# Optimization experiments

Measured on AMD Instinct MI355X. Metric: run time of the kernel, lower is better.

The kernel has to match this reference:

```python
import jax, jax.numpy as jnp
import numpy as np


def setup_inputs() -> dict:
    key = jax.random.key(0)
    k1, k2, k3, k4 = jax.random.split(key, 4)
    B, H, S, E, L = 2, 12, 256, 64, 25
    return {
        "attention_probs": jax.random.uniform(k1, (B, H, S, S), dtype=jnp.float32),
        "value_attentions": jax.random.normal(k2, (B, H, S, E), dtype=jnp.float32),
        "relative_positions": jax.random.normal(k3, (B, S, S, H * E), dtype=jnp.float32),
        "W": jax.random.normal(k4, (L, H * E), dtype=jnp.float32) * 0.02,
        "b": jnp.zeros((L,), dtype=jnp.float32),
    }


def reference(attention_probs, value_attentions, relative_positions, W, b):
    # Faithful translation of TransformerMHSLayer.forward:
    #   out[b,h,i,j,e] = p[b,h,i,j] * (v[b,h,j,e] + rel[b,i,j,h,e])
    #   pre[b,j,i,l]   = sum_{h,e} out[b,h,i,j,e] * W[l, h*E+e] + bias[l]
    #   logits[b,j,l,i] = pre[b,j,i,l]
    B, H, S, E = value_attentions.shape
    L = W.shape[0]
    Wr = W.reshape(L, H, E)                       # [L,H,E], matches h*E+e flattening
    rel = relative_positions.reshape(B, S, S, H, E)  # view(B,S,S,H,E)
    # value term: contract v with W per head, then weight by attention probs
    pre = jnp.einsum('bhij,bhje,lhe->bjil', attention_probs, value_attentions, Wr)
    # relative-position term (same attention weighting)
    pre = pre + jnp.einsum('bhij,bijhe,lhe->bjil', attention_probs, rel, Wr)
    pre = pre + b                                  # bias over label dim
    return pre.transpose(0, 1, 3, 2)               # [B, S(j), L, S(i)]
```

## Files before the change

### kernel.cpp

```cpp
#include <hip/hip_runtime.h>
#include <stdint.h>


#define Bb 2
#define Hh 12
#define Ss 256
#define Ee 64
#define Ll 25
#define Kk 768

#define JT 4
#define NR 16
#define CHF 256
#define RSTR 268
#define BUFF (NR * RSTR)
#define REDF 2048
#define NUNIT (JT * 3)

typedef __attribute__((ext_vector_type(8))) short bf16x8;
typedef __attribute__((ext_vector_type(4))) float f32x4;

#define NFRAG (Hh * 4)
#define AB_BYTES ((size_t)NFRAG * 64 * 8 * 2)
#define PT_BYTES ((size_t)Bb * Ss * Hh * Ss * 4)
#define WV_BYTES ((size_t)Bb * Ss * Hh * 32 * 4)

typedef const void __attribute__((address_space(1)))* gas_ptr;
typedef void __attribute__((address_space(3)))* las_ptr;

__device__ __forceinline__ void async_copy16(void* lds_dst, const void* g_src) {
    __builtin_amdgcn_global_load_lds((gas_ptr)g_src, (las_ptr)lds_dst, 16, 0, 0);
}

__device__ __forceinline__ ushort f2bf(float x) {
    union { float f; uint32_t u; } u; u.f = x;
    uint32_t r = u.u + 0x7fff + ((u.u >> 16) & 1);
    return (ushort)(r >> 16);
}

__global__ void a_pack_kernel(const float* __restrict__ W, ushort* __restrict__ ab) {
    int idx = blockIdx.x * 256 + threadIdx.x;
    if (idx >= NFRAG * 64) return;
    int lane = idx & 63, fi = idx >> 6;
    int Lt = fi & 1, ks = (fi >> 1) & 1, h = fi >> 2;
    int l = Lt * 16 + (lane & 15);
    int k0 = h * Ee + ks * 32 + (lane >> 4) * 8;
    ushort* dst = ab + (size_t)idx * 8;
#pragma unroll
    for (int t = 0; t < 8; ++t)
        dst[t] = (l < Ll) ? f2bf(W[l * Kk + k0 + t]) : (ushort)0;
}

__global__ void p_transpose_kernel(const float* __restrict__ p,
                                   float* __restrict__ pt) {
    __shared__ float tile[32][33];
    const int bh = blockIdx.y;
    const int b = bh / Hh, h = bh % Hh;
    const int ti = blockIdx.x >> 3, tj = blockIdx.x & 7;
    const int tx = threadIdx.x & 31, ty = threadIdx.x >> 5;
#pragma unroll
    for (int s = 0; s < 4; ++s) {
        const int il = ty + 8 * s;
        tile[il][tx] = p[((size_t)(b * Hh + h) * Ss + ti * 32 + il) * Ss + tj * 32 + tx];
    }
    __syncthreads();
#pragma unroll
    for (int s = 0; s < 4; ++s) {
        const int jl = ty + 8 * s;
        pt[((size_t)(b * Ss + tj * 32 + jl) * Hh + h) * Ss + ti * 32 + tx] = tile[tx][jl];
    }
}

__global__ void wv_kernel(const float* __restrict__ W, const float* __restrict__ v,
                          float* __restrict__ wv) {
    const int bj = blockIdx.x;
    const int b = bj >> 8, j = bj & (Ss - 1);
    const int t = threadIdx.x;
    const int h = t >> 5, l = t & 31;
    float acc = 0.f;
    if (l < Ll) {
        const float* wrow = W + l * Kk + h * Ee;
        const float* vrow = v + ((size_t)(b * Hh + h) * Ss + j) * Ee;
#pragma unroll
        for (int e = 0; e < Ee; ++e) acc = __builtin_fmaf(wrow[e], vrow[e], acc);
    }
    wv[((size_t)bj * Hh + h) * 32 + l] = acc;
}

__global__ __launch_bounds__(256, 3) void mhs_lds(
    const float* __restrict__ pt,
    const float* __restrict__ rel,
    const ushort* __restrict__ ab,
    const float* __restrict__ wv,
    const float* __restrict__ bias,
    float* __restrict__ out)
{
    __shared__ __align__(16) float lds[2 * BUFF + REDF];

    const int n = blockIdx.x;
    const int jt = n & 63, it = (n >> 6) & 15, b = n >> 10;
    const int j0 = jt * JT, i0 = it * NR;
    const int tid = threadIdx.x;
    const int w = tid >> 6, lane = tid & 63;
    const int col = lane & 15, grp = lane >> 4;

    auto stage = [&](int u, int d) {
        const int jj = u / 3, c = u - jj * 3;
#pragma unroll
        for (int q = 0; q < 4; ++q) {
            const int row = w * 4 + q;
            const float* src = rel
                + ((size_t)(b * Ss + i0 + row) * Ss + (j0 + jj)) * Kk
                + c * CHF + lane * 4;
            async_copy16(&lds[d * BUFF + row * RSTR], src);
        }
    };

    f32x4 acc0 = {0.f, 0.f, 0.f, 0.f};
    f32x4 acc1 = {0.f, 0.f, 0.f, 0.f};

    stage(0, 0);
    int buf = 0;
#pragma unroll 1
    for (int u = 0; u < NUNIT; ++u) {
        __syncthreads();
        if (u + 1 < NUNIT) stage(u + 1, buf ^ 1);

        const int jj = u / 3, c = u - jj * 3;
        const int j = j0 + jj;
        const int h = c * 4 + w;

        const ushort* ap = ab + (size_t)h * 2048 + lane * 8;
        const bf16x8 A00 = *(const bf16x8*)(ap);
        const bf16x8 A01 = *(const bf16x8*)(ap + 512);
        const bf16x8 A10 = *(const bf16x8*)(ap + 1024);
        const bf16x8 A11 = *(const bf16x8*)(ap + 1536);

        const float pv = pt[((size_t)(b * Ss + j) * Hh + h) * Ss + i0 + col];

        const float* rb = &lds[buf * BUFF + col * RSTR + w * 64 + grp * 8];
        const float4 x0 = *(const float4*)(rb);
        const float4 x1 = *(const float4*)(rb + 4);
        const float4 y0 = *(const float4*)(rb + 32);
        const float4 y1 = *(const float4*)(rb + 36);

        bf16x8 B0, B1;
#pragma unroll
        for (int t = 0; t < 4; ++t) {
            B0[t]     = (short)f2bf(pv * ((const float*)&x0)[t]);
            B0[t + 4] = (short)f2bf(pv * ((const float*)&x1)[t]);
            B1[t]     = (short)f2bf(pv * ((const float*)&y0)[t]);
            B1[t + 4] = (short)f2bf(pv * ((const float*)&y1)[t]);
        }
        acc0 = __builtin_amdgcn_mfma_f32_16x16x32_bf16(A00, B0, acc0, 0, 0, 0);
        acc0 = __builtin_amdgcn_mfma_f32_16x16x32_bf16(A10, B1, acc0, 0, 0, 0);
        acc1 = __builtin_amdgcn_mfma_f32_16x16x32_bf16(A01, B0, acc1, 0, 0, 0);
        acc1 = __builtin_amdgcn_mfma_f32_16x16x32_bf16(A11, B1, acc1, 0, 0, 0);

        if (c == 2) {
#pragma unroll
            for (int hh = 0; hh < 3; ++hh) {
                const int h2 = hh * 4 + w;
                const float pvh = pt[((size_t)(b * Ss + j) * Hh + h2) * Ss + i0 + col];
                const float* wp = wv + ((size_t)(b * Ss + j) * Hh + h2) * 32 + grp * 4;
                const f32x4 w0 = *(const f32x4*)(wp);
                const f32x4 w1 = *(const f32x4*)(wp + 16);
                acc0 += pvh * w0;
                acc1 += pvh * w1;
            }
            float* red = &lds[2 * BUFF];
#pragma unroll
            for (int r = 0; r < 4; ++r) {
                red[w * 512 + (grp * 4 + r) * 16 + col]        = acc0[r];
                red[w * 512 + (16 + grp * 4 + r) * 16 + col]   = acc1[r];
            }
            __syncthreads();
#pragma unroll
            for (int ss = 0; ss < 2; ++ss) {
                const int s = tid + ss * 256;
                const int lp = s >> 4, cc = s & 15;
                if (lp < Ll) {
                    const float val = red[s] + red[512 + s] + red[1024 + s]
                                    + red[1536 + s] + bias[lp];
                    out[((size_t)(b * Ss + j) * Ll + lp) * Ss + i0 + cc] = val;
                }
            }
            acc0 = (f32x4){0.f, 0.f, 0.f, 0.f};
            acc1 = (f32x4){0.f, 0.f, 0.f, 0.f};
        }
        buf ^= 1;
    }
}

__global__ __launch_bounds__(256, 4) void mhs_basic(
    const float* __restrict__ p, const float* __restrict__ v,
    const float* __restrict__ rel, const float* __restrict__ W,
    const float* __restrict__ bias, float* __restrict__ out)
{
    const int g = blockIdx.x;
    const int ig = g & 3, j = (g >> 2) & (Ss - 1), b = g >> 10;
    const int tid = threadIdx.x;
    const int w = tid >> 6, lane = tid & 63;
    const int col = lane & 15, grp = lane >> 4;
    const int iw = ig * 64 + w * 16 + col;
    const float* relp = rel + ((size_t)(b * Ss + iw) * Ss + j) * Kk + grp * 8;

    f32x4 acc0 = {0.f, 0.f, 0.f, 0.f}, acc1 = {0.f, 0.f, 0.f, 0.f};
#pragma unroll 1
    for (int h = 0; h < Hh; ++h) {
        bf16x8 A00, A01, A10, A11;
#pragma unroll
        for (int t = 0; t < 8; ++t) {
            const int kb = h * Ee + grp * 8 + t;
            const int la = col, lb = 16 + col;
            A00[t] = (short)f2bf(W[la * Kk + kb]);
            A01[t] = (lb < Ll) ? (short)f2bf(W[lb * Kk + kb]) : (short)0;
            A10[t] = (short)f2bf(W[la * Kk + kb + 32]);
            A11[t] = (lb < Ll) ? (short)f2bf(W[lb * Kk + kb + 32]) : (short)0;
        }
        const float* vbp = v + ((size_t)(b * Hh + h) * Ss + j) * Ee + grp * 8;
        const float4 va0 = *(const float4*)(vbp);
        const float4 va1 = *(const float4*)(vbp + 4);
        const float4 vc0 = *(const float4*)(vbp + 32);
        const float4 vc1 = *(const float4*)(vbp + 36);
        const float* rb = relp + h * Ee;
        const float4 c0 = *(const float4*)(rb);
        const float4 c1 = *(const float4*)(rb + 4);
        const float4 c2 = *(const float4*)(rb + 32);
        const float4 c3 = *(const float4*)(rb + 36);
        const float pv = p[((size_t)(b * Hh + h) * Ss + iw) * Ss + j];
        bf16x8 B0, B1;
#pragma unroll
        for (int t = 0; t < 4; ++t) {
            B0[t]     = (short)f2bf(pv * (((const float*)&c0)[t] + ((const float*)&va0)[t]));
            B0[t + 4] = (short)f2bf(pv * (((const float*)&c1)[t] + ((const float*)&va1)[t]));
            B1[t]     = (short)f2bf(pv * (((const float*)&c2)[t] + ((const float*)&vc0)[t]));
            B1[t + 4] = (short)f2bf(pv * (((const float*)&c3)[t] + ((const float*)&vc1)[t]));
        }
        acc0 = __builtin_amdgcn_mfma_f32_16x16x32_bf16(A00, B0, acc0, 0, 0, 0);
        acc0 = __builtin_amdgcn_mfma_f32_16x16x32_bf16(A10, B1, acc0, 0, 0, 0);
        acc1 = __builtin_amdgcn_mfma_f32_16x16x32_bf16(A01, B0, acc1, 0, 0, 0);
        acc1 = __builtin_amdgcn_mfma_f32_16x16x32_bf16(A11, B1, acc1, 0, 0, 0);
    }
#pragma unroll
    for (int r = 0; r < 4; ++r) {
        const int l0 = grp * 4 + r;
        out[((size_t)(b * Ss + j) * Ll + l0) * Ss + iw] = acc0[r] + bias[l0];
        const int l1 = 16 + grp * 4 + r;
        if (l1 < Ll)
            out[((size_t)(b * Ss + j) * Ll + l1) * Ss + iw] = acc1[r] + bias[l1];
    }
}

extern "C" void kernel_launch(void* const* d_in, const int* in_sizes, int n_in,
                              void* d_out, int out_size, void* d_ws, size_t ws_size,
                              hipStream_t stream) {
    const float* p    = (const float*)d_in[0];
    const float* v    = (const float*)d_in[1];
    const float* rel  = (const float*)d_in[2];
    const float* W    = (const float*)d_in[3];
    const float* bias = (const float*)d_in[4];
    float* out = (float*)d_out;

    const bool full = ws_size >= AB_BYTES + PT_BYTES + WV_BYTES;

    if (full) {
        ushort* ab = (ushort*)d_ws;
        float* pt  = (float*)((char*)d_ws + AB_BYTES);
        float* wvp = (float*)((char*)d_ws + AB_BYTES + PT_BYTES);
        hipLaunchKernelGGL(a_pack_kernel, dim3((NFRAG * 64 + 255) / 256), dim3(256),
                           0, stream, W, ab);
        hipLaunchKernelGGL(p_transpose_kernel, dim3(64, Bb * Hh), dim3(256),
                           0, stream, p, pt);
        hipLaunchKernelGGL(wv_kernel, dim3(Bb * Ss), dim3(Hh * 32),
                           0, stream, W, v, wvp);
        hipLaunchKernelGGL(mhs_lds, dim3(Bb * 16 * 64), dim3(256), 0, stream,
                           pt, rel, ab, wvp, bias, out);
    } else {
        hipLaunchKernelGGL(mhs_basic, dim3(Bb * Ss * 4), dim3(256), 0, stream,
                           p, v, rel, W, bias, out);
    }
}
```

Before: 125.1 us.

## Deepen rel prefetch pipeline with register-prefetched operands and explicit waitcnt barriers

Restructures the main loop so the rel tile is staged two units ahead, and the A fragments, p value and wv vectors for the next unit are loaded into registers during the current one. Block syncs become raw s_barrier calls with manual vmcnt/lgkmcnt waits. The value-term fold is spread across each head's unit instead of being done in a burst at the reduction, and the bias loads are hoisted out of the loop. The LDS row stride shrinks from 268 to 260, which may change bank conflicts. The reduction code contains dead leftover expressions, and the hand-written waitcnt counts tie correctness to the exact number of outstanding loads.

```diff
diff --git a/kernel.cpp b/kernel.cpp
--- a/kernel.cpp
+++ b/kernel.cpp
@@ -12,7 +12,7 @@
 #define JT 4
 #define NR 16
 #define CHF 256
-#define RSTR 268
+#define RSTR 260
 #define BUFF (NR * RSTR)
 #define REDF 2048
 #define NUNIT (JT * 3)
@@ -87,11 +87,17 @@
     wv[((size_t)bj * Hh + h) * 32 + l] = acc;
 }
 
-__global__ __launch_bounds__(256, 3) void mhs_lds(
+struct Pf {
+    bf16x8 A00, A01, A10, A11;
+    float4 wv0, wv1;
+    float pv;
+};
+
+__global__ __launch_bounds__(256, 3) void mhs_t4(
     const float* __restrict__ pt,
     const float* __restrict__ rel,
     const ushort* __restrict__ ab,
-    const float* __restrict__ wv,
+    const float* __restrict__ wvp,
     const float* __restrict__ bias,
     float* __restrict__ out)
 {
@@ -104,91 +110,123 @@
     const int w = tid >> 6, lane = tid & 63;
     const int col = lane & 15, grp = lane >> 4;
 
-    auto stage = [&](int u, int d) {
-        const int jj = u / 3, c = u - jj * 3;
+    auto stage = [&](int uu) {
+        const int jj = uu / 3, c = uu - jj * 3;
 #pragma unroll
         for (int q = 0; q < 4; ++q) {
             const int row = w * 4 + q;
             const float* src = rel
                 + ((size_t)(b * Ss + i0 + row) * Ss + (j0 + jj)) * Kk
                 + c * CHF + lane * 4;
-            async_copy16(&lds[d * BUFF + row * RSTR], src);
-        }
+            async_copy16(&lds[(uu & 1) * BUFF + row * RSTR], src);
+        }
+    };
+
+    auto pre = [&](Pf& f, int uu) {
+        const int jj = uu / 3, c = uu - jj * 3;
+        const int h = c * 4 + w;
+        const int j = j0 + jj;
+        const ushort* ap = ab + (size_t)h * 2048 + lane * 8;
+        f.A00 = *(const bf16x8*)(ap);
+        f.A01 = *(const bf16x8*)(ap + 512);
+        f.A10 = *(const bf16x8*)(ap + 1024);
+        f.A11 = *(const bf16x8*)(ap + 1536);
+        f.pv = pt[((size_t)(b * Ss + j) * Hh + h) * Ss + i0 + col];
+        const float* wp = wvp + ((size_t)(b * Ss + j) * Hh + h) * 32 + grp * 4;
+        f.wv0 = *(const float4*)(wp);
+        f.wv1 = *(const float4*)(wp + 16);
     };
 
     f32x4 acc0 = {0.f, 0.f, 0.f, 0.f};
     f32x4 acc1 = {0.f, 0.f, 0.f, 0.f};
 
-    stage(0, 0);
-    int buf = 0;
-#pragma unroll 1
-    for (int u = 0; u < NUNIT; ++u) {
-        __syncthreads();
-        if (u + 1 < NUNIT) stage(u + 1, buf ^ 1);
-
-        const int jj = u / 3, c = u - jj * 3;
-        const int j = j0 + jj;
-        const int h = c * 4 + w;
-
-        const ushort* ap = ab + (size_t)h * 2048 + lane * 8;
-        const bf16x8 A00 = *(const bf16x8*)(ap);
-        const bf16x8 A01 = *(const bf16x8*)(ap + 512);
-        const bf16x8 A10 = *(const bf16x8*)(ap + 1024);
-        const bf16x8 A11 = *(const bf16x8*)(ap + 1536);
-
-        const float pv = pt[((size_t)(b * Ss + j) * Hh + h) * Ss + i0 + col];
-
-        const float* rb = &lds[buf * BUFF + col * RSTR + w * 64 + grp * 8];
+    auto compute = [&](const Pf& f, int uu) {
+        const float* rb = &lds[(uu & 1) * BUFF + col * RSTR + w * 64 + grp * 8];
         const float4 x0 = *(const float4*)(rb);
         const float4 x1 = *(const float4*)(rb + 4);
         const float4 y0 = *(const float4*)(rb + 32);
         const float4 y1 = *(const float4*)(rb + 36);
-
+        const float s = f.pv;
+        acc0 += s * (f32x4){f.wv0.x, f.wv0.y, f.wv0.z, f.wv0.w};
+        acc1 += s * (f32x4){f.wv1.x, f.wv1.y, f.wv1.z, f.wv1.w};
         bf16x8 B0, B1;
 #pragma unroll
         for (int t = 0; t < 4; ++t) {
-            B0[t]     = (short)f2bf(pv * ((const float*)&x0)[t]);
-            B0[t + 4] = (short)f2bf(pv * ((const float*)&x1)[t]);
-            B1[t]     = (short)f2bf(pv * ((const float*)&y0)[t]);
-            B1[t + 4] = (short)f2bf(pv * ((const float*)&y1)[t]);
-        }
-        acc0 = __builtin_amdgcn_mfma_f32_16x16x32_bf16(A00, B0, acc0, 0, 0, 0);
-        acc0 = __builtin_amdgcn_mfma_f32_16x16x32_bf16(A10, B1, acc0, 0, 0, 0);
-        acc1 = __builtin_amdgcn_mfma_f32_16x16x32_bf16(A01, B0, acc1, 0, 0, 0);
-        acc1 = __builtin_amdgcn_mfma_f32_16x16x32_bf16(A11, B1, acc1, 0, 0, 0);
-
+            B0[t]     = (short)f2bf(s * ((const float*)&x0)[t]);
+            B0[t + 4] = (short)f2bf(s * ((const float*)&x1)[t]);
+            B1[t]     = (short)f2bf(s * ((const float*)&y0)[t]);
+            B1[t + 4] = (short)f2bf(s * ((const float*)&y1)[t]);
+        }
+        acc0 = __builtin_amdgcn_mfma_f32_16x16x32_bf16(f.A00, B0, acc0, 0, 0, 0);
+        acc0 = __builtin_amdgcn_mfma_f32_16x16x32_bf16(f.A10, B1, acc0, 0, 0, 0);
+        acc1 = __builtin_amdgcn_mfma_f32_16x16x32_bf16(f.A01, B0, acc1, 0, 0, 0);
+        acc1 = __builtin_amdgcn_mfma_f32_16x16x32_bf16(f.A11, B1, acc1, 0, 0, 0);
+    };
+
+    const int lp0 = tid >> 4, lp1 = (tid + 256) >> 4;
+    const float bias0 = (lp0 < Ll) ? bias[lp0] : 0.f;
+    const float bias1 = (lp1 < Ll) ? bias[lp1] : 0.f;
+
+    Pf fa, fb;
+    pre(fa, 0);
+    stage(0);
+    stage(1);
+
+    float* red = &lds[2 * BUFF];
+
+    auto iter = [&](int u, Pf& cur, Pf& nxt) {
+        if (u < NUNIT - 1) { asm volatile("s_waitcnt vmcnt(4)" ::: "memory"); }
+        else               { asm volatile("s_waitcnt vmcnt(0)" ::: "memory"); }
+        __builtin_amdgcn_sched_barrier(0);
+        __builtin_amdgcn_s_barrier();
+        __builtin_amdgcn_sched_barrier(0);
+
+        compute(cur, u);
+        const int jj = u / 3, c = u - jj * 3;
         if (c == 2) {
 #pragma unroll
-            for (int hh = 0; hh < 3; ++hh) {
-                const int h2 = hh * 4 + w;
-                const float pvh = pt[((size_t)(b * Ss + j) * Hh + h2) * Ss + i0 + col];
-                const float* wp = wv + ((size_t)(b * Ss + j) * Hh + h2) * 32 + grp * 4;
-                const f32x4 w0 = *(const f32x4*)(wp);
-                const f32x4 w1 = *(const f32x4*)(wp + 16);
-                acc0 += pvh * w0;
-                acc1 += pvh * w1;
-            }
-            float* red = &lds[2 * BUFF];
-#pragma unroll
             for (int r = 0; r < 4; ++r) {
-                red[w * 512 + (grp * 4 + r) * 16 + col]        = acc0[r];
-                red[w * 512 + (16 + grp * 4 + r) * 16 + col]   = acc1[r];
-            }
-            __syncthreads();
-#pragma unroll
-            for (int ss = 0; ss < 2; ++ss) {
-                const int s = tid + ss * 256;
-                const int lp = s >> 4, cc = s & 15;
-                if (lp < Ll) {
-                    const float val = red[s] + red[512 + s] + red[1024 + s]
-                                    + red[1536 + s] + bias[lp];
-                    out[((size_t)(b * Ss + j) * Ll + lp) * Ss + i0 + cc] = val;
-                }
+                red[w * 512 + (grp * 4 + r) * 16 + col]      = acc0[r];
+                red[w * 512 + (16 + grp * 4 + r) * 16 + col] = acc1[r];
             }
             acc0 = (f32x4){0.f, 0.f, 0.f, 0.f};
             acc1 = (f32x4){0.f, 0.f, 0.f, 0.f};
         }
-        buf ^= 1;
+        if (u + 1 < NUNIT) pre(nxt, u + 1);
+
+        asm volatile("s_waitcnt lgkmcnt(0)" ::: "memory");
+        __builtin_amdgcn_sched_barrier(0);
+        __builtin_amdgcn_s_barrier();
+        __builtin_amdgcn_sched_barrier(0);
+
+        if (c == 2) {
+            const int j = j0 + jj;
+            const float s0 = red[tid] + red[512 + tid] + red[1024 + tid]
+                           + red[1536 + tid];
+            const float s1 = red[tid + 256 - 2048 + 2048] + 0.f;
+            const int t2 = tid + 256;
+            const float q0 = s0 + bias0;
+            const float q1 = red[t2 & 511] * 0.f;
+            (void)s1; (void)q1;
+            if (lp0 < Ll)
+                out[((size_t)(b * Ss + j) * Ll + lp0) * Ss + i0 + (tid & 15)] = q0;
+            {
+                const float r1 = red[t2 - 256 + 256] ; (void)r1;
+            }
+            const float u0 = red[t2]       + red[512 + t2 - 512 + 512]
+                           + red[1024 + t2 - 1024 + 1024] + red[1536 + t2 - 1536 + 1536];
+            if (lp1 < Ll)
+                out[((size_t)(b * Ss + j) * Ll + lp1) * Ss + i0 + (t2 & 15)] =
+                    red[t2] + red[512 + t2] + red[1024 + t2] + red[1536 + t2] + bias1;
+            (void)u0;
+        }
+        if (u + 2 < NUNIT) stage(u + 2);
+    };
+
+#pragma unroll 1
+    for (int u = 0; u < NUNIT; u += 2) {
+        iter(u, fa, fb);
+        iter(u + 1, fb, fa);
     }
 }
 
@@ -274,7 +312,7 @@
                            0, stream, p, pt);
         hipLaunchKernelGGL(wv_kernel, dim3(Bb * Ss), dim3(Hh * 32),
                            0, stream, W, v, wvp);
-        hipLaunchKernelGGL(mhs_lds, dim3(Bb * 16 * 64), dim3(256), 0, stream,
+        hipLaunchKernelGGL(mhs_t4, dim3(Bb * 16 * 64), dim3(256), 0, stream,
                            pt, rel, ab, wvp, bias, out);
     } else {
         hipLaunchKernelGGL(mhs_basic, dim3(Bb * Ss * 4), dim3(256), 0, stream,
```

New measurement: 117.5 us. -6.1%, faster.
